# Performance work log

Measured on AMD Instinct MI355X. Metric: run time of the kernel, lower is better.

Reference implementation:

```python
import jax, jax.numpy as jnp
import numpy as np

KS = 3          # kernel_size
DILS = (1, 2)   # dilation list
NH = 8          # num_heads


def _unfold(x, k, r):
    # x: [B, d, H, W] -> [B, d, k*k, H, W], matching nn.Unfold(k, dilation=r,
    # padding=r*(k-1)//2): kernel positions enumerated row-major over (kh, kw).
    B, d, H, W = x.shape
    pad = r * (k - 1) // 2
    xp = jnp.pad(x, ((0, 0), (0, 0), (pad, pad), (pad, pad)))
    patches = [xp[:, :, i * r:i * r + H, j * r:j * r + W]
               for i in range(k) for j in range(k)]
    return jnp.stack(patches, axis=2)


def setup_inputs() -> dict:
    key = jax.random.key(0)
    k1, k2, k3, k4 = jax.random.split(key, 4)
    B, H, W, C = 2, 160, 160, 128
    return {
        "x": jax.random.normal(k1, (B, H, W, C), dtype=jnp.float32),
        "qkv_w": jax.random.normal(k2, (3 * C, C), dtype=jnp.float32) * 0.05,
        "proj_w": jax.random.normal(k3, (C, C), dtype=jnp.float32) * 0.05,
        "proj_b": jax.random.normal(k4, (C,), dtype=jnp.float32) * 0.05,
    }


def reference(x, qkv_w, proj_w, proj_b):
    B, H, W, C = x.shape
    nd = len(DILS)
    hd = C // NH               # head_dim = 16
    d = C // nd                # channels per dilation group = 64
    h = d // hd                # heads per dilation group = 4
    scale = hd ** -0.5
    L = H * W

    xc = x.transpose(0, 3, 1, 2)                       # [B, C, H, W]
    qkv = jnp.einsum('bchw,oc->bohw', xc, qkv_w)       # 1x1 conv, no bias
    qkv = qkv.reshape(B, 3, nd, d, H, W)

    outs = []
    for i, r in enumerate(DILS):
        q, kk, v = qkv[:, 0, i], qkv[:, 1, i], qkv[:, 2, i]   # [B, d, H, W]
        qh = q.reshape(B, h, hd, L).transpose(0, 1, 3, 2)      # [B, h, L, hd]
        ku = _unfold(kk, KS, r).reshape(B, h, hd, KS * KS, L)  # [B, h, hd, 9, L]
        vu = _unfold(v, KS, r).reshape(B, h, hd, KS * KS, L)
        attn = jnp.einsum('bhld,bhdkl->bhlk', qh, ku) * scale  # [B, h, L, 9]
        attn = jax.nn.softmax(attn, axis=-1)
        o = jnp.einsum('bhlk,bhdkl->bhld', attn, vu)           # [B, h, L, hd]
        outs.append(o.transpose(0, 2, 1, 3).reshape(B, H, W, d))

    y = jnp.concatenate(outs, axis=-1)                  # [B, H, W, C]
    return y @ proj_w.T + proj_b
```

## Files before the change

### kernel.cpp

```cpp
#include <hip/hip_runtime.h>
#include <cstdint>

#define HW_ 160
#define NPIX (2*160*160)

typedef __attribute__((ext_vector_type(8))) short short8;
typedef __attribute__((ext_vector_type(4))) float f32x4;

__device__ __forceinline__ unsigned short f2bf(float f) {
  union { float f; unsigned u; } v; v.f = f;
  unsigned r = v.u + 0x7fffu + ((v.u >> 16) & 1u);
  return (unsigned short)(r >> 16);
}
__device__ __forceinline__ float bflo(unsigned u) {
  union { unsigned u; float f; } v; v.u = u << 16; return v.f;
}
__device__ __forceinline__ float bfhi(unsigned u) {
  union { unsigned u; float f; } v; v.u = u & 0xffff0000u; return v.f;
}

__device__ __forceinline__ short8 cvt8(const float4& x0, const float4& x1) {
  short8 h;
  h[0] = (short)f2bf(x0.x); h[1] = (short)f2bf(x0.y);
  h[2] = (short)f2bf(x0.z); h[3] = (short)f2bf(x0.w);
  h[4] = (short)f2bf(x1.x); h[5] = (short)f2bf(x1.y);
  h[6] = (short)f2bf(x1.z); h[7] = (short)f2bf(x1.w);
  return h;
}

__global__ __launch_bounds__(256)
void cvt_w(const float* __restrict__ qw, unsigned short* __restrict__ dst) {
  int i = (blockIdx.x * 256 + threadIdx.x) * 4;
  float4 v = *(const float4*)(qw + i);
  dst[i] = f2bf(v.x); dst[i + 1] = f2bf(v.y);
  dst[i + 2] = f2bf(v.z); dst[i + 3] = f2bf(v.w);
}

__global__ __launch_bounds__(256, 4)
void qkv_gemm(const float* __restrict__ x, const unsigned short* __restrict__ wq,
              uint2* __restrict__ qt4) {
  const int t = threadIdx.x;
  const int lane = t & 63, wv = t >> 6;
  const int wp = wv & 1, wc = wv >> 1;
  const int lr = lane & 15, lk = lane >> 4;
  const int p0 = blockIdx.x * 64;
  const int o0 = blockIdx.y * 64 + wc * 32;

  short8 bfr[2][4];
#pragma unroll
  for (int n = 0; n < 2; ++n) {
    const unsigned short* wr_ = wq + (size_t)(o0 + n * 16 + lr) * 128 + lk * 8;
#pragma unroll
    for (int kk = 0; kk < 4; ++kk)
      bfr[n][kk] = *(const short8*)(wr_ + kk * 32);
  }

  short8 af[2][4];
#pragma unroll
  for (int m = 0; m < 2; ++m) {
    const float* xp = x + (size_t)(p0 + wp * 32 + m * 16 + lr) * 128 + lk * 8;
#pragma unroll
    for (int kk = 0; kk < 4; ++kk) {
      float4 a0 = *(const float4*)(xp + kk * 32);
      float4 a1 = *(const float4*)(xp + kk * 32 + 4);
      af[m][kk] = cvt8(a0, a1);
    }
  }

  f32x4 acc[2][2];
#pragma unroll
  for (int n = 0; n < 2; ++n)
#pragma unroll
    for (int m = 0; m < 2; ++m) acc[n][m] = 0.f;
#pragma unroll
  for (int kk = 0; kk < 4; ++kk)
#pragma unroll
    for (int n = 0; n < 2; ++n)
#pragma unroll
      for (int m = 0; m < 2; ++m)
        acc[n][m] = __builtin_amdgcn_mfma_f32_16x16x32_bf16(
            bfr[n][kk], af[m][kk], acc[n][m], 0, 0, 0);

#pragma unroll
  for (int n = 0; n < 2; ++n)
#pragma unroll
    for (int m = 0; m < 2; ++m) {
      int ob = o0 + n * 16 + lk * 4;
      int p = p0 + wp * 32 + m * 16 + lr;
      uint2 u;
      u.x = ((unsigned)f2bf(acc[n][m][1]) << 16) | f2bf(acc[n][m][0]);
      u.y = ((unsigned)f2bf(acc[n][m][3]) << 16) | f2bf(acc[n][m][2]);
      qt4[(size_t)(ob >> 2) * NPIX + p] = u;
    }
}

__global__ __launch_bounds__(512, 4)
void attn_proj(const uint2* __restrict__ qt4,
               const float* __restrict__ wp_f32,
               const float* __restrict__ bias, float* __restrict__ C) {
  __shared__ short Ys[64 * 128];
  __shared__ short Ws[128 * 128];
  const int t = threadIdx.x;
  const int p0 = blockIdx.x * 64;

#pragma unroll
  for (int i = 0; i < 4; ++i) {
    int f = t + i * 512;
    int row = f >> 4;
    float4 x0 = *(const float4*)(wp_f32 + f * 8);
    float4 x1 = *(const float4*)(wp_f32 + f * 8 + 4);
    int dst = (row * 256 + (f & 15) * 16) ^ ((row & 7) << 4);
    *(short8*)((char*)Ws + dst) = cvt8(x0, x1);
  }

  const int lane = t & 63, wv = t >> 6;
  const int dil = wv >> 2, head = wv & 3;
  const int r = dil ? 2 : 1;
  const int p = p0 + lane;
  const int rem = p % (HW_ * HW_);
  const int yy = rem / HW_;
  const int xx = rem - yy * HW_;
  const int brow4 = dil * 16 + head * 4;

  const uint2* qp = qt4 + (size_t)brow4 * NPIX + p;
  float q[16];
#pragma unroll
  for (int c4 = 0; c4 < 4; ++c4) {
    uint2 u = qp[(size_t)c4 * NPIX];
    q[4 * c4]     = bflo(u.x); q[4 * c4 + 1] = bfhi(u.x);
    q[4 * c4 + 2] = bflo(u.y); q[4 * c4 + 3] = bfhi(u.y);
  }

  int np[9];
  bool val[9];
#pragma unroll
  for (int jy = 0; jy < 3; ++jy)
#pragma unroll
    for (int jx = 0; jx < 3; ++jx) {
      const int j = jy * 3 + jx;
      const int dy = (jy - 1) * r, dx = (jx - 1) * r;
      val[j] = ((unsigned)(yy + dy) < HW_) && ((unsigned)(xx + dx) < HW_);
      int q_ = p + dy * HW_ + dx;
      np[j] = min(max(q_, 0), NPIX - 1);
    }

  float l[9];
#pragma unroll
  for (int j = 0; j < 9; ++j) l[j] = 0.f;
  const uint2* kp = qt4 + (size_t)(32 + brow4) * NPIX;
#pragma unroll
  for (int c4 = 0; c4 < 4; ++c4) {
    const uint2* rp = kp + (size_t)c4 * NPIX;
    const float qa = q[4 * c4], qb = q[4 * c4 + 1];
    const float qc = q[4 * c4 + 2], qd = q[4 * c4 + 3];
#pragma unroll
    for (int j = 0; j < 9; ++j) {
      uint2 u = rp[np[j]];
      l[j] += qa * bflo(u.x) + qb * bfhi(u.x) + qc * bflo(u.y) + qd * bfhi(u.y);
    }
  }
#pragma unroll
  for (int j = 0; j < 9; ++j) l[j] = val[j] ? l[j] * 0.25f : 0.f;

  float mx = l[0];
#pragma unroll
  for (int j = 1; j < 9; ++j) mx = fmaxf(mx, l[j]);
  float e[9], s = 0.f;
#pragma unroll
  for (int j = 0; j < 9; ++j) { e[j] = __expf(l[j] - mx); s += e[j]; }
#pragma unroll
  for (int j = 0; j < 9; ++j) if (!val[j]) e[j] = 0.f;
  const float inv = 1.0f / s;

  float o[16];
#pragma unroll
  for (int c = 0; c < 16; ++c) o[c] = 0.f;
  const uint2* vp = qt4 + (size_t)(64 + brow4) * NPIX;
#pragma unroll
  for (int c4 = 0; c4 < 4; ++c4) {
    const uint2* rp = vp + (size_t)c4 * NPIX;
#pragma unroll
    for (int j = 0; j < 9; ++j) {
      uint2 u = rp[np[j]];
      o[4 * c4]     += e[j] * bflo(u.x);
      o[4 * c4 + 1] += e[j] * bfhi(u.x);
      o[4 * c4 + 2] += e[j] * bflo(u.y);
      o[4 * c4 + 3] += e[j] * bfhi(u.y);
    }
  }

  {
    short8 h0, h1;
#pragma unroll
    for (int c = 0; c < 8; ++c) h0[c] = (short)f2bf(o[c] * inv);
#pragma unroll
    for (int c = 0; c < 8; ++c) h1[c] = (short)f2bf(o[c + 8] * inv);
    int colb = (dil * 64 + head * 16) * 2;
    int base = (lane * 256 + colb) ^ ((lane & 7) << 4);
    *(short8*)((char*)Ys + base) = h0;
    int base2 = (lane * 256 + colb + 16) ^ ((lane & 7) << 4);
    *(short8*)((char*)Ys + base2) = h1;
  }
  __syncthreads();

  const int wq_ = wv & 3, wo = wv >> 2;
  const int lr = lane & 15, lk = lane >> 4;

  short8 a[4];
#pragma unroll
  for (int kk = 0; kk < 4; ++kk) {
    int row = wq_ * 16 + lr;
    int off = (row * 256 + kk * 64 + lk * 16) ^ ((row & 7) << 4);
    a[kk] = *(const short8*)((const char*)Ys + off);
  }

  f32x4 acc[4];
#pragma unroll
  for (int n = 0; n < 4; ++n) acc[n] = 0.f;
#pragma unroll
  for (int kk = 0; kk < 4; ++kk) {
    short8 b[4];
#pragma unroll
    for (int n = 0; n < 4; ++n) {
      int row = wo * 64 + n * 16 + lr;
      int off = (row * 256 + kk * 64 + lk * 16) ^ ((row & 7) << 4);
      b[n] = *(const short8*)((const char*)Ws + off);
    }
#pragma unroll
    for (int n = 0; n < 4; ++n)
      acc[n] = __builtin_amdgcn_mfma_f32_16x16x32_bf16(a[kk], b[n], acc[n], 0, 0, 0);
  }

#pragma unroll
  for (int n = 0; n < 4; ++n) {
    int ccol = wo * 64 + n * 16 + lr;
    float bv = bias[ccol];
    int crow = p0 + wq_ * 16 + lk * 4;
#pragma unroll
    for (int i = 0; i < 4; ++i)
      C[(size_t)(crow + i) * 128 + ccol] = acc[n][i] + bv;
  }
}

extern "C" void kernel_launch(void* const* d_in, const int* in_sizes, int n_in,
                              void* d_out, int out_size, void* d_ws, size_t ws_size,
                              hipStream_t stream) {
  const float* x      = (const float*)d_in[0];
  const float* qkv_w  = (const float*)d_in[1];
  const float* proj_w = (const float*)d_in[2];
  const float* proj_b = (const float*)d_in[3];
  float* out = (float*)d_out;

  uint2* qt4 = (uint2*)d_ws;
  unsigned short* wqbf = (unsigned short*)(qt4 + (size_t)96 * NPIX);

  cvt_w<<<48, 256, 0, stream>>>(qkv_w, wqbf);

  qkv_gemm<<<dim3(NPIX / 64, 6), 256, 0, stream>>>(x, wqbf, qt4);

  attn_proj<<<NPIX / 64, 512, 0, stream>>>(qt4, proj_w, proj_b, out);
}
```

Before: 157.3 us.

## Pre-convert x to bf16 and stage via LDS, reuse across 192 outputs

The conversion kernel now also converts the input activations x to bf16 in the workspace. The QKV GEMM loads a bf16 x tile into LDS through direct global-to-LDS loads and computes three 64-wide output chunks per block (grid y shrinks from 6 to 2). Before, each of the six column blocks re-read the full fp32 x tile, so this cuts redundant activation reads. The cost is an extra fp32-read and bf16-write pass over x in the conversion kernel, plus lower occupancy and fewer GEMM blocks.

Result: faster. 134.4 us (-14.5%).

```diff
diff --git a/kernel.cpp b/kernel.cpp
--- a/kernel.cpp
+++ b/kernel.cpp
@@ -29,69 +29,114 @@
 }
 
 __global__ __launch_bounds__(256)
-void cvt_w(const float* __restrict__ qw, unsigned short* __restrict__ dst) {
+void cvt_all(const float* __restrict__ qw, const float* __restrict__ x,
+             unsigned short* __restrict__ wdst, unsigned short* __restrict__ xdst) {
   int i = (blockIdx.x * 256 + threadIdx.x) * 4;
-  float4 v = *(const float4*)(qw + i);
-  dst[i] = f2bf(v.x); dst[i + 1] = f2bf(v.y);
-  dst[i + 2] = f2bf(v.z); dst[i + 3] = f2bf(v.w);
-}
-
-__global__ __launch_bounds__(256, 4)
-void qkv_gemm(const float* __restrict__ x, const unsigned short* __restrict__ wq,
+  if (i < 49152) {
+    float4 v = *(const float4*)(qw + i);
+    ushort4 h;
+    h.x = f2bf(v.x); h.y = f2bf(v.y); h.z = f2bf(v.z); h.w = f2bf(v.w);
+    *(ushort4*)(wdst + i) = h;
+  } else {
+    int j = i - 49152;
+    float4 v = *(const float4*)(x + j);
+    ushort4 h;
+    h.x = f2bf(v.x); h.y = f2bf(v.y); h.z = f2bf(v.z); h.w = f2bf(v.w);
+    *(ushort4*)(xdst + j) = h;
+  }
+}
+
+__global__ __launch_bounds__(256, 3)
+void qkv_gemm(const unsigned short* __restrict__ xbf,
+              const unsigned short* __restrict__ wq,
               uint2* __restrict__ qt4) {
+  __shared__ short As[64 * 128];
   const int t = threadIdx.x;
+  const int p0 = blockIdx.x * 64;
+  const int og = blockIdx.y;
+
   const int lane = t & 63, wv = t >> 6;
   const int wp = wv & 1, wc = wv >> 1;
   const int lr = lane & 15, lk = lane >> 4;
-  const int p0 = blockIdx.x * 64;
-  const int o0 = blockIdx.y * 64 + wc * 32;
-
-  short8 bfr[2][4];
-#pragma unroll
-  for (int n = 0; n < 2; ++n) {
-    const unsigned short* wr_ = wq + (size_t)(o0 + n * 16 + lr) * 128 + lk * 8;
+
+  const unsigned short* wbase =
+      wq + (size_t)(og * 192 + wc * 32 + lr) * 128 + lk * 8;
+  short8 bfr0[2][4];
+#pragma unroll
+  for (int n = 0; n < 2; ++n)
 #pragma unroll
     for (int kk = 0; kk < 4; ++kk)
-      bfr[n][kk] = *(const short8*)(wr_ + kk * 32);
-  }
+      bfr0[n][kk] = *(const short8*)(wbase + n * 16 * 128 + kk * 32);
+
+  {
+    const char* gx = (const char*)(xbf + (size_t)p0 * 128);
+#pragma unroll
+    for (int i = 0; i < 4; ++i) {
+      int f = i * 256 + t;
+      int row = f >> 4;
+      int src = (f * 16) ^ ((row & 7) << 4);
+      __builtin_amdgcn_global_load_lds(
+          (const __attribute__((address_space(1))) unsigned int*)(gx + src),
+          (__attribute__((address_space(3))) unsigned int*)
+              ((char*)As + i * 4096 + wv * 1024),
+          16, 0, 0);
+    }
+  }
+  __syncthreads();
 
   short8 af[2][4];
 #pragma unroll
-  for (int m = 0; m < 2; ++m) {
-    const float* xp = x + (size_t)(p0 + wp * 32 + m * 16 + lr) * 128 + lk * 8;
+  for (int m = 0; m < 2; ++m)
 #pragma unroll
     for (int kk = 0; kk < 4; ++kk) {
-      float4 a0 = *(const float4*)(xp + kk * 32);
-      float4 a1 = *(const float4*)(xp + kk * 32 + 4);
-      af[m][kk] = cvt8(a0, a1);
-    }
-  }
-
-  f32x4 acc[2][2];
-#pragma unroll
-  for (int n = 0; n < 2; ++n)
-#pragma unroll
-    for (int m = 0; m < 2; ++m) acc[n][m] = 0.f;
-#pragma unroll
-  for (int kk = 0; kk < 4; ++kk)
+      int row = wp * 32 + m * 16 + lr;
+      int off = (row * 256 + kk * 64 + lk * 16) ^ ((row & 7) << 4);
+      af[m][kk] = *(const short8*)((const char*)As + off);
+    }
+
+#pragma unroll
+  for (int it = 0; it < 3; ++it) {
+    short8 bfr[2][4];
+    if (it == 0) {
+#pragma unroll
+      for (int n = 0; n < 2; ++n)
+#pragma unroll
+        for (int kk = 0; kk < 4; ++kk) bfr[n][kk] = bfr0[n][kk];
+    } else {
+#pragma unroll
+      for (int n = 0; n < 2; ++n)
+#pragma unroll
+        for (int kk = 0; kk < 4; ++kk)
+          bfr[n][kk] = *(const short8*)(wbase + (it * 64 + n * 16) * 128 + kk * 32);
+    }
+
+    f32x4 acc[2][2];
 #pragma unroll
     for (int n = 0; n < 2; ++n)
 #pragma unroll
-      for (int m = 0; m < 2; ++m)
-        acc[n][m] = __builtin_amdgcn_mfma_f32_16x16x32_bf16(
-            bfr[n][kk], af[m][kk], acc[n][m], 0, 0, 0);
-
-#pragma unroll
-  for (int n = 0; n < 2; ++n)
-#pragma unroll
-    for (int m = 0; m < 2; ++m) {
-      int ob = o0 + n * 16 + lk * 4;
-      int p = p0 + wp * 32 + m * 16 + lr;
-      uint2 u;
-      u.x = ((unsigned)f2bf(acc[n][m][1]) << 16) | f2bf(acc[n][m][0]);
-      u.y = ((unsigned)f2bf(acc[n][m][3]) << 16) | f2bf(acc[n][m][2]);
-      qt4[(size_t)(ob >> 2) * NPIX + p] = u;
-    }
+      for (int m = 0; m < 2; ++m) acc[n][m] = 0.f;
+#pragma unroll
+    for (int kk = 0; kk < 4; ++kk)
+#pragma unroll
+      for (int n = 0; n < 2; ++n)
+#pragma unroll
+        for (int m = 0; m < 2; ++m)
+          acc[n][m] = __builtin_amdgcn_mfma_f32_16x16x32_bf16(
+              bfr[n][kk], af[m][kk], acc[n][m], 0, 0, 0);
+
+    const int o0 = og * 192 + it * 64 + wc * 32;
+#pragma unroll
+    for (int n = 0; n < 2; ++n)
+#pragma unroll
+      for (int m = 0; m < 2; ++m) {
+        int ob = o0 + n * 16 + lk * 4;
+        int p = p0 + wp * 32 + m * 16 + lr;
+        uint2 u;
+        u.x = ((unsigned)f2bf(acc[n][m][1]) << 16) | f2bf(acc[n][m][0]);
+        u.y = ((unsigned)f2bf(acc[n][m][3]) << 16) | f2bf(acc[n][m][2]);
+        qt4[(size_t)(ob >> 2) * NPIX + p] = u;
+      }
+  }
 }
 
 __global__ __launch_bounds__(512, 4)
@@ -253,10 +298,11 @@
 
   uint2* qt4 = (uint2*)d_ws;
   unsigned short* wqbf = (unsigned short*)(qt4 + (size_t)96 * NPIX);
-
-  cvt_w<<<48, 256, 0, stream>>>(qkv_w, wqbf);
-
-  qkv_gemm<<<dim3(NPIX / 64, 6), 256, 0, stream>>>(x, wqbf, qt4);
+  unsigned short* xbf  = wqbf + 49152;
+
+  cvt_all<<<6448, 256, 0, stream>>>(qkv_w, x, wqbf, xbf);
+
+  qkv_gemm<<<dim3(NPIX / 64, 2), 256, 0, stream>>>(xbf, wqbf, qt4);
 
   attn_proj<<<NPIX / 64, 512, 0, stream>>>(qt4, proj_w, proj_b, out);
 }
```

## Retile QKV GEMM to 128-pixel blocks with LDS-staged bf16 activations

Applied to the files above, without the earlier changes.

The QKV projection now uses 512-thread blocks covering 128 pixels and 192 output channels. Each block loads and converts x to bf16 once into swizzled LDS, and each wave loops over three 32-channel output chunks. Before, x was reread and reconverted for each of the 6 output-channel blocks, so this cuts global reads of x from 6x to 2x per pixel. In exchange it adds 32KB of LDS per block, higher register pressure from the preloaded weight fragments, and a block-wide barrier. The weight conversion kernel also now writes its four bf16 values with one vector store.

After: 134.2 us. 1.17x faster.

```diff
diff --git a/kernel.cpp b/kernel.cpp
--- a/kernel.cpp
+++ b/kernel.cpp
@@ -32,66 +32,91 @@
 void cvt_w(const float* __restrict__ qw, unsigned short* __restrict__ dst) {
   int i = (blockIdx.x * 256 + threadIdx.x) * 4;
   float4 v = *(const float4*)(qw + i);
-  dst[i] = f2bf(v.x); dst[i + 1] = f2bf(v.y);
-  dst[i + 2] = f2bf(v.z); dst[i + 3] = f2bf(v.w);
-}
-
-__global__ __launch_bounds__(256, 4)
+  ushort4 h;
+  h.x = f2bf(v.x); h.y = f2bf(v.y); h.z = f2bf(v.z); h.w = f2bf(v.w);
+  *(ushort4*)(dst + i) = h;
+}
+
+__global__ __launch_bounds__(512, 2)
 void qkv_gemm(const float* __restrict__ x, const unsigned short* __restrict__ wq,
               uint2* __restrict__ qt4) {
+  __shared__ short As[128 * 128];
   const int t = threadIdx.x;
+  const int p0 = blockIdx.x * 128;
+  const int og = blockIdx.y;
+
   const int lane = t & 63, wv = t >> 6;
-  const int wp = wv & 1, wc = wv >> 1;
+  const int wpx = wv & 3, wo = wv >> 2;
   const int lr = lane & 15, lk = lane >> 4;
-  const int p0 = blockIdx.x * 64;
-  const int o0 = blockIdx.y * 64 + wc * 32;
-
-  short8 bfr[2][4];
-#pragma unroll
-  for (int n = 0; n < 2; ++n) {
-    const unsigned short* wr_ = wq + (size_t)(o0 + n * 16 + lr) * 128 + lk * 8;
+
+  const float* A = x + (size_t)p0 * 128;
+  float4 xr[4][2];
+#pragma unroll
+  for (int i = 0; i < 4; ++i) {
+    int f = t + i * 512;
+    xr[i][0] = *(const float4*)(A + f * 8);
+    xr[i][1] = *(const float4*)(A + f * 8 + 4);
+  }
+
+  const unsigned short* wbase =
+      wq + (size_t)(og * 192 + wo * 96 + lr) * 128 + lk * 8;
+  short8 bfr[3][2][4];
+#pragma unroll
+  for (int it = 0; it < 3; ++it)
+#pragma unroll
+    for (int n = 0; n < 2; ++n)
+#pragma unroll
+      for (int kk = 0; kk < 4; ++kk)
+        bfr[it][n][kk] = *(const short8*)(wbase + (it * 32 + n * 16) * 128 + kk * 32);
+
+#pragma unroll
+  for (int i = 0; i < 4; ++i) {
+    int f = t + i * 512;
+    int row = f >> 4;
+    int dst = (row * 256 + (f & 15) * 16) ^ ((row & 7) << 4);
+    *(short8*)((char*)As + dst) = cvt8(xr[i][0], xr[i][1]);
+  }
+  __syncthreads();
+
+  short8 af[2][4];
+#pragma unroll
+  for (int m = 0; m < 2; ++m)
+#pragma unroll
+    for (int kk = 0; kk < 4; ++kk) {
+      int row = wpx * 32 + m * 16 + lr;
+      int off = (row * 256 + kk * 64 + lk * 16) ^ ((row & 7) << 4);
+      af[m][kk] = *(const short8*)((const char*)As + off);
+    }
+
+#pragma unroll
+  for (int it = 0; it < 3; ++it) {
+    f32x4 acc[2][2];
+#pragma unroll
+    for (int n = 0; n < 2; ++n)
+#pragma unroll
+      for (int m = 0; m < 2; ++m) acc[n][m] = 0.f;
 #pragma unroll
     for (int kk = 0; kk < 4; ++kk)
-      bfr[n][kk] = *(const short8*)(wr_ + kk * 32);
-  }
-
-  short8 af[2][4];
-#pragma unroll
-  for (int m = 0; m < 2; ++m) {
-    const float* xp = x + (size_t)(p0 + wp * 32 + m * 16 + lr) * 128 + lk * 8;
-#pragma unroll
-    for (int kk = 0; kk < 4; ++kk) {
-      float4 a0 = *(const float4*)(xp + kk * 32);
-      float4 a1 = *(const float4*)(xp + kk * 32 + 4);
-      af[m][kk] = cvt8(a0, a1);
-    }
-  }
-
-  f32x4 acc[2][2];
-#pragma unroll
-  for (int n = 0; n < 2; ++n)
-#pragma unroll
-    for (int m = 0; m < 2; ++m) acc[n][m] = 0.f;
-#pragma unroll
-  for (int kk = 0; kk < 4; ++kk)
+#pragma unroll
+      for (int n = 0; n < 2; ++n)
+#pragma unroll
+        for (int m = 0; m < 2; ++m)
+          acc[n][m] = __builtin_amdgcn_mfma_f32_16x16x32_bf16(
+              bfr[it][n][kk], af[m][kk], acc[n][m], 0, 0, 0);
+
+    const int o0 = og * 192 + wo * 96 + it * 32;
 #pragma unroll
     for (int n = 0; n < 2; ++n)
 #pragma unroll
-      for (int m = 0; m < 2; ++m)
-        acc[n][m] = __builtin_amdgcn_mfma_f32_16x16x32_bf16(
-            bfr[n][kk], af[m][kk], acc[n][m], 0, 0, 0);
-
-#pragma unroll
-  for (int n = 0; n < 2; ++n)
-#pragma unroll
-    for (int m = 0; m < 2; ++m) {
-      int ob = o0 + n * 16 + lk * 4;
-      int p = p0 + wp * 32 + m * 16 + lr;
-      uint2 u;
-      u.x = ((unsigned)f2bf(acc[n][m][1]) << 16) | f2bf(acc[n][m][0]);
-      u.y = ((unsigned)f2bf(acc[n][m][3]) << 16) | f2bf(acc[n][m][2]);
-      qt4[(size_t)(ob >> 2) * NPIX + p] = u;
-    }
+      for (int m = 0; m < 2; ++m) {
+        int ob = o0 + n * 16 + lk * 4;
+        int p = p0 + wpx * 32 + m * 16 + lr;
+        uint2 u;
+        u.x = ((unsigned)f2bf(acc[n][m][1]) << 16) | f2bf(acc[n][m][0]);
+        u.y = ((unsigned)f2bf(acc[n][m][3]) << 16) | f2bf(acc[n][m][2]);
+        qt4[(size_t)(ob >> 2) * NPIX + p] = u;
+      }
+  }
 }
 
 __global__ __launch_bounds__(512, 4)
@@ -256,7 +281,7 @@
 
   cvt_w<<<48, 256, 0, stream>>>(qkv_w, wqbf);
 
-  qkv_gemm<<<dim3(NPIX / 64, 6), 256, 0, stream>>>(x, wqbf, qt4);
+  qkv_gemm<<<dim3(NPIX / 128, 2), 512, 0, stream>>>(x, wqbf, qt4);
 
   attn_proj<<<NPIX / 64, 512, 0, stream>>>(qt4, proj_w, proj_b, out);
 }
```
